# Kernel tuning notes

Measured on AMD Instinct MI355X. Metric: run time of the kernel, lower is better.

## Reference

```python
import jax, jax.numpy as jnp
import numpy as np

B, S, I, Hd = 64, 512, 512, 1024


def setup_inputs() -> dict:
    key = jax.random.key(0)
    ks = jax.random.split(key, 13)
    stdv = 1.0 / np.sqrt(Hd)
    u = lambda k, shp: jax.random.uniform(k, shp, jnp.float32, -stdv, stdv)
    x = jax.random.normal(ks[0], (B, S, I), jnp.float32)
    names = {}
    i = 1
    for g in ('1', '2', '3', '4'):
        names['X' + g] = u(ks[i], (I, Hd)); i += 1
        names['H' + g] = u(ks[i], (Hd, Hd)); i += 1
        names['b' + g] = u(ks[i], (Hd,)); i += 1
    return dict(x=x, **names)


def _lstm_forward(x, X1, H1, b1, X2, H2, b2, X3, H3, b3, X4, H4, b4):
    # Fuse the four input projections into one GEMM; math identical to
    # computing each x_t @ Xk + bk separately (slices of the concat).
    Xcat = jnp.concatenate([X1, X2, X3, X4], axis=1)          # [I, 4H]
    Hcat = jnp.concatenate([H1, H2, H3, H4], axis=1)          # [H, 4H]
    bcat = jnp.concatenate([b1, b2, b3, b4])                  # [4H]
    xg = jnp.einsum('bsi,ig->bsg', x, Xcat) + bcat            # [B, S, 4H]
    xg = jnp.swapaxes(xg, 0, 1)                               # [S, B, 4H] for scan

    Bsz = x.shape[0]
    h0 = jnp.zeros((Bsz, Hd), x.dtype)
    c0 = jnp.zeros((Bsz, Hd), x.dtype)

    def step(carry, xg_t):
        h, c = carry
        g = xg_t + h @ Hcat                                   # [B, 4H]
        s1 = jax.nn.sigmoid(g[:, :Hd])        # forget gate
        s2 = jax.nn.sigmoid(g[:, Hd:2 * Hd])  # input gate
        t1 = jnp.tanh(g[:, 2 * Hd:3 * Hd])    # candidate
        s3 = jax.nn.sigmoid(g[:, 3 * Hd:])    # output gate
        c = c * s1 + s2 * t1
        h = jnp.tanh(c) * s3
        return (h, c), h

    _, hs = jax.lax.scan(step, (h0, c0), xg)                  # hs: [S, B, H]
    return jnp.swapaxes(hs, 0, 1)                             # [B, S, H]


def reference(x, X1, H1, b1, X2, H2, b2, X3, H3, b3, X4, H4, b4):
    return _lstm_forward(x, X1, H1, b1, X2, H2, b2, X3, H3, b3, X4, H4, b4)
```

## Files before the change

### kernel.cpp

```cpp
#include <hip/hip_runtime.h>
#include <stdint.h>
#include <stddef.h>

typedef __attribute__((ext_vector_type(8))) short bf16x8;
typedef __attribute__((ext_vector_type(4))) float f32x4;

#define NBLK 128
#define NTHR 512
#define S_LEN 512
#define HD   1024
#define IDIM 512

#define MFMA16 __builtin_amdgcn_mfma_f32_16x16x32_bf16

__device__ __forceinline__ float bf2f(uint16_t u){
  union { uint32_t i; float f; } v; v.i = ((uint32_t)u) << 16; return v.f;
}
__device__ __forceinline__ uint16_t f2bf(float f){
  union { float f; uint32_t i; } v; v.f = f;
  uint32_t r = v.i + 0x7fffu + ((v.i >> 16) & 1u);
  return (uint16_t)(r >> 16);
}
__device__ __forceinline__ float sigm(float x){ return 1.0f / (1.0f + __expf(-x)); }
__device__ __forceinline__ float tanh_(float x){
  float t = fminf(fmaxf(2.0f * x, -30.0f), 30.0f);
  float e = __expf(t);
  return (e - 1.0f) / (e + 1.0f);
}

__device__ __forceinline__ void split8(const float* p, bf16x8& hi8, bf16x8& lo8){
  const float4 a = *(const float4*)p;
  const float4 b = *(const float4*)(p + 4);
  float v[8] = {a.x, a.y, a.z, a.w, b.x, b.y, b.z, b.w};
  #pragma unroll
  for (int j = 0; j < 8; ++j){
    uint16_t h = f2bf(v[j]);
    hi8[j] = (short)h;
    lo8[j] = (short)f2bf(v[j] - bf2f(h));
  }
}

__device__ __forceinline__ void cload16(const uint16_t* p, bf16x8& d){
  asm volatile("global_load_dwordx4 %0, %1, off sc0 sc1" : "=v"(d) : "v"(p));
}
__device__ __forceinline__ void cstore16b(uint16_t* p, uint32_t v){
  asm volatile("global_store_short %0, %1, off sc0 sc1" :: "v"(p), "v"(v) : "memory");
}

__global__ void __launch_bounds__(NTHR, 2) lstm_persist(
    const float* __restrict__ x,
    const float* __restrict__ X1, const float* __restrict__ H1, const float* __restrict__ b1,
    const float* __restrict__ X2, const float* __restrict__ H2, const float* __restrict__ b2,
    const float* __restrict__ X3, const float* __restrict__ H3, const float* __restrict__ b3,
    const float* __restrict__ X4, const float* __restrict__ H4, const float* __restrict__ b4,
    float* __restrict__ out, uint16_t* hbhi, uint16_t* hblo, int* done)
{
  __shared__ float part[8][64][36];
  const int tid  = threadIdx.x;
  const int w    = tid >> 6;
  const int L    = tid & 63;
  const int c    = L & 15;
  const int quad = L >> 4;
  const int cc   = c & 7;
  const int f    = blockIdx.x;
  const int colh = f * 8 + cc;
  const bool hiHalf = (c >= 8);

  const float* W0 = hiHalf ? H2 : H1;
  const float* W1 = hiHalf ? H4 : H3;
  const float* V0 = hiHalf ? X2 : X1;
  const float* V1 = hiHalf ? X4 : X3;
  const float bias0 = (hiHalf ? b2 : b1)[colh];
  const float bias1 = (hiHalf ? b4 : b3)[colh];

  bf16x8 BhH0[4], BhL0[4], BhH1[4], BhL1[4];
  #pragma unroll
  for (int kk = 0; kk < 4; ++kk){
    const int kb = w*128 + kk*32 + quad*8;
    bf16x8 h0, l0, h1, l1;
    #pragma unroll
    for (int j = 0; j < 8; ++j){
      float w0 = W0[(size_t)(kb + j)*HD + colh];
      uint16_t a = f2bf(w0); h0[j] = (short)a; l0[j] = (short)f2bf(w0 - bf2f(a));
      float w1 = W1[(size_t)(kb + j)*HD + colh];
      uint16_t b_ = f2bf(w1); h1[j] = (short)b_; l1[j] = (short)f2bf(w1 - bf2f(b_));
    }
    BhH0[kk] = h0; BhL0[kk] = l0; BhH1[kk] = h1; BhL1[kk] = l1;
  }
  bf16x8 BxH0[2], BxL0[2], BxH1[2], BxL1[2];
  #pragma unroll
  for (int kk = 0; kk < 2; ++kk){
    const int kb = w*64 + kk*32 + quad*8;
    bf16x8 h0, l0, h1, l1;
    #pragma unroll
    for (int j = 0; j < 8; ++j){
      float w0 = V0[(size_t)(kb + j)*HD + colh];
      uint16_t a = f2bf(w0); h0[j] = (short)a; l0[j] = (short)f2bf(w0 - bf2f(a));
      float w1 = V1[(size_t)(kb + j)*HD + colh];
      uint16_t b_ = f2bf(w1); h1[j] = (short)b_; l1[j] = (short)f2bf(w1 - bf2f(b_));
    }
    BxH0[kk] = h0; BxL0[kk] = l0; BxH1[kk] = h1; BxL1[kk] = l1;
  }

  float cst[2] = {0.f, 0.f};

  #pragma unroll 1
  for (int t = 0; t < S_LEN; ++t){
    const int p = t & 1;
    f32x4 acc0[4], acc1[4];
    #pragma unroll
    for (int m = 0; m < 4; ++m){
      acc0[m] = (f32x4){0.f,0.f,0.f,0.f};
      acc1[m] = (f32x4){0.f,0.f,0.f,0.f};
    }

    #pragma unroll
    for (int kk = 0; kk < 2; ++kk){
      #pragma unroll
      for (int m = 0; m < 4; ++m){
        const float* xp = x + ((size_t)(16*m + c)*S_LEN + t)*IDIM + w*64 + kk*32 + quad*8;
        bf16x8 Ah, Al; split8(xp, Ah, Al);
        acc0[m] = MFMA16(Ah, BxH0[kk], acc0[m], 0, 0, 0);
        acc0[m] = MFMA16(Al, BxH0[kk], acc0[m], 0, 0, 0);
        acc0[m] = MFMA16(Ah, BxL0[kk], acc0[m], 0, 0, 0);
        acc1[m] = MFMA16(Ah, BxH1[kk], acc1[m], 0, 0, 0);
        acc1[m] = MFMA16(Al, BxH1[kk], acc1[m], 0, 0, 0);
        acc1[m] = MFMA16(Ah, BxL1[kk], acc1[m], 0, 0, 0);
      }
    }

    if (t > 0){
      if (tid < NBLK){
        while (__hip_atomic_load(&done[tid*32], __ATOMIC_RELAXED, __HIP_MEMORY_SCOPE_AGENT) < t)
          __builtin_amdgcn_s_sleep(1);
      }
      __syncthreads();
    }

    const uint16_t* hbH = hbhi + (size_t)p * (64*HD);
    const uint16_t* hbL = hblo + (size_t)p * (64*HD);
    {
      bf16x8 AH[2][4], AL[2][4];
      #define H_OFF(m, kk) ((size_t)(16*(m) + c)*HD + w*128 + (kk)*32 + quad*8)
      #define ISSUE_M(buf, m) do { \
        _Pragma("unroll") \
        for (int kk = 0; kk < 4; ++kk){ \
          cload16(hbH + H_OFF(m, kk), AH[buf][kk]); \
          cload16(hbL + H_OFF(m, kk), AL[buf][kk]); \
        } } while(0)

      asm volatile("s_waitcnt vmcnt(0)" ::: "memory");
      ISSUE_M(0, 0);
      #pragma unroll
      for (int m = 0; m < 4; ++m){
        const int buf = m & 1;
        if (m < 3){
          ISSUE_M(buf ^ 1, m + 1);
          asm volatile("s_waitcnt vmcnt(8)" ::: "memory");
        } else {
          asm volatile("s_waitcnt vmcnt(0)" ::: "memory");
        }
        __builtin_amdgcn_sched_barrier(0);
        #pragma unroll
        for (int kk = 0; kk < 4; ++kk){
          acc0[m] = MFMA16(AH[buf][kk], BhH0[kk], acc0[m], 0, 0, 0);
          acc0[m] = MFMA16(AL[buf][kk], BhH0[kk], acc0[m], 0, 0, 0);
          acc0[m] = MFMA16(AH[buf][kk], BhL0[kk], acc0[m], 0, 0, 0);
          acc1[m] = MFMA16(AH[buf][kk], BhH1[kk], acc1[m], 0, 0, 0);
          acc1[m] = MFMA16(AL[buf][kk], BhH1[kk], acc1[m], 0, 0, 0);
          acc1[m] = MFMA16(AH[buf][kk], BhL1[kk], acc1[m], 0, 0, 0);
        }
      }
      #undef ISSUE_M
      #undef H_OFF
    }

    #pragma unroll
    for (int m = 0; m < 4; ++m){
      #pragma unroll
      for (int r = 0; r < 4; ++r){
        part[w][16*m + quad*4 + r][c]      = acc0[m][r];
        part[w][16*m + quad*4 + r][16 + c] = acc1[m][r];
      }
    }
    __syncthreads();

    float g0[2], g1[2];
    #pragma unroll
    for (int r2 = 0; r2 < 2; ++r2){
      const int row = 8*w + quad*2 + r2;
      float a = bias0, b = bias1;
      #pragma unroll
      for (int ww = 0; ww < 8; ++ww){
        a += part[ww][row][c];
        b += part[ww][row][16 + c];
      }
      g0[r2] = a; g1[r2] = b;
    }

    uint16_t* hwH = hbhi + (size_t)(p^1) * (64*HD);
    uint16_t* hwL = hblo + (size_t)(p^1) * (64*HD);
    float hv[2];
    #pragma unroll
    for (int r2 = 0; r2 < 2; ++r2){
      float gf = g0[r2];
      float gi = __shfl_xor(g0[r2], 8, 64);
      float gc = g1[r2];
      float go = __shfl_xor(g1[r2], 8, 64);
      float cn = cst[r2] * sigm(gf) + sigm(gi) * tanh_(gc);
      cst[r2] = cn;
      hv[r2] = tanh_(cn) * sigm(go);
    }
    if (!hiHalf){
      #pragma unroll
      for (int r2 = 0; r2 < 2; ++r2){
        const int batch = 8*w + quad*2 + r2;
        uint16_t hh = f2bf(hv[r2]);
        uint16_t hl = f2bf(hv[r2] - bf2f(hh));
        cstore16b(hwH + (size_t)batch*HD + colh, (uint32_t)hh);
        cstore16b(hwL + (size_t)batch*HD + colh, (uint32_t)hl);
      }
    }

    asm volatile("s_waitcnt vmcnt(0)" ::: "memory");
    __syncthreads();
    if (tid == 0)
      __hip_atomic_store(&done[f*32], t + 1, __ATOMIC_RELAXED, __HIP_MEMORY_SCOPE_AGENT);

    if (!hiHalf){
      #pragma unroll
      for (int r2 = 0; r2 < 2; ++r2){
        const int batch = 8*w + quad*2 + r2;
        __builtin_nontemporal_store(hv[r2], &out[(size_t)(batch*S_LEN + t)*HD + colh]);
      }
    }
  }
}

extern "C" void kernel_launch(void* const* d_in, const int* in_sizes, int n_in,
                              void* d_out, int out_size, void* d_ws, size_t ws_size,
                              hipStream_t stream) {
  const float* x  = (const float*)d_in[0];
  const float* X1 = (const float*)d_in[1];
  const float* H1 = (const float*)d_in[2];
  const float* b1 = (const float*)d_in[3];
  const float* X2 = (const float*)d_in[4];
  const float* H2 = (const float*)d_in[5];
  const float* b2 = (const float*)d_in[6];
  const float* X3 = (const float*)d_in[7];
  const float* H3 = (const float*)d_in[8];
  const float* b3 = (const float*)d_in[9];
  const float* X4 = (const float*)d_in[10];
  const float* H4 = (const float*)d_in[11];
  const float* b4 = (const float*)d_in[12];
  float* out = (float*)d_out;

  uint16_t* hbhi = (uint16_t*)d_ws;
  uint16_t* hblo = (uint16_t*)((char*)d_ws + 262144);
  int* done      = (int*)((char*)d_ws + 524288);
  hipMemsetAsync(d_ws, 0, 524288 + 16384, stream);

  hipLaunchKernelGGL(lstm_persist, dim3(NBLK), dim3(NTHR), 0, stream,
                     x, X1, H1, b1, X2, H2, b2, X3, H3, b3, X4, H4, b4,
                     out, hbhi, hblo, done);
}
```

Measured before the change: 7.554 ms.

## Move input projection after barrier and interleave x loads with h-loads pipeline

The x-projection MFMAs, which do not depend on h, move from before the inter-block wait to after it. Their x loads are now issued by hand and interleaved with the double-buffered h loads and recurrent MFMAs, so both load streams share one vmcnt-driven pipeline. The apparent aim is to hide global load latency inside the critical path after the wait. The trade-off is that x-projection work that used to overlap with waiting on other blocks now sits on the serial path after the barrier, and register pressure rises. The spin sleep interval is also doubled.

```diff
diff --git a/kernel.cpp b/kernel.cpp
--- a/kernel.cpp
+++ b/kernel.cpp
@@ -28,10 +28,9 @@
   return (e - 1.0f) / (e + 1.0f);
 }
 
-__device__ __forceinline__ void split8(const float* p, bf16x8& hi8, bf16x8& lo8){
-  const float4 a = *(const float4*)p;
-  const float4 b = *(const float4*)(p + 4);
-  float v[8] = {a.x, a.y, a.z, a.w, b.x, b.y, b.z, b.w};
+__device__ __forceinline__ void split8v(const f32x4& a, const f32x4& b,
+                                        bf16x8& hi8, bf16x8& lo8){
+  float v[8] = {a[0], a[1], a[2], a[3], b[0], b[1], b[2], b[3]};
   #pragma unroll
   for (int j = 0; j < 8; ++j){
     uint16_t h = f2bf(v[j]);
@@ -43,9 +42,17 @@
 __device__ __forceinline__ void cload16(const uint16_t* p, bf16x8& d){
   asm volatile("global_load_dwordx4 %0, %1, off sc0 sc1" : "=v"(d) : "v"(p));
 }
+__device__ __forceinline__ void nload16(const float* p, f32x4& d){
+  asm volatile("global_load_dwordx4 %0, %1, off" : "=v"(d) : "v"(p));
+}
 __device__ __forceinline__ void cstore16b(uint16_t* p, uint32_t v){
   asm volatile("global_store_short %0, %1, off sc0 sc1" :: "v"(p), "v"(v) : "memory");
 }
+
+#define WAITV(n) do { \
+    asm volatile("s_waitcnt vmcnt(" #n ")" ::: "memory"); \
+    __builtin_amdgcn_sched_barrier(0); \
+  } while (0)
 
 __global__ void __launch_bounds__(NTHR, 2) lstm_persist(
     const float* __restrict__ x,
@@ -114,75 +121,98 @@
       acc1[m] = (f32x4){0.f,0.f,0.f,0.f};
     }
 
-    #pragma unroll
-    for (int kk = 0; kk < 2; ++kk){
-      #pragma unroll
-      for (int m = 0; m < 4; ++m){
-        const float* xp = x + ((size_t)(16*m + c)*S_LEN + t)*IDIM + w*64 + kk*32 + quad*8;
-        bf16x8 Ah, Al; split8(xp, Ah, Al);
-        acc0[m] = MFMA16(Ah, BxH0[kk], acc0[m], 0, 0, 0);
-        acc0[m] = MFMA16(Al, BxH0[kk], acc0[m], 0, 0, 0);
-        acc0[m] = MFMA16(Ah, BxL0[kk], acc0[m], 0, 0, 0);
-        acc1[m] = MFMA16(Ah, BxH1[kk], acc1[m], 0, 0, 0);
-        acc1[m] = MFMA16(Al, BxH1[kk], acc1[m], 0, 0, 0);
-        acc1[m] = MFMA16(Ah, BxL1[kk], acc1[m], 0, 0, 0);
-      }
-    }
-
     if (t > 0){
       if (tid < NBLK){
         while (__hip_atomic_load(&done[tid*32], __ATOMIC_RELAXED, __HIP_MEMORY_SCOPE_AGENT) < t)
-          __builtin_amdgcn_s_sleep(1);
+          __builtin_amdgcn_s_sleep(2);
       }
       __syncthreads();
     }
 
     const uint16_t* hbH = hbhi + (size_t)p * (64*HD);
     const uint16_t* hbL = hblo + (size_t)p * (64*HD);
-    {
-      bf16x8 AH[2][4], AL[2][4];
-      #define H_OFF(m, kk) ((size_t)(16*(m) + c)*HD + w*128 + (kk)*32 + quad*8)
-      #define ISSUE_M(buf, m) do { \
-        _Pragma("unroll") \
-        for (int kk = 0; kk < 4; ++kk){ \
-          cload16(hbH + H_OFF(m, kk), AH[buf][kk]); \
-          cload16(hbL + H_OFF(m, kk), AL[buf][kk]); \
-        } } while(0)
-
-      asm volatile("s_waitcnt vmcnt(0)" ::: "memory");
-      ISSUE_M(0, 0);
-      #pragma unroll
-      for (int m = 0; m < 4; ++m){
-        const int buf = m & 1;
-        if (m < 3){
-          ISSUE_M(buf ^ 1, m + 1);
-          asm volatile("s_waitcnt vmcnt(8)" ::: "memory");
-        } else {
-          asm volatile("s_waitcnt vmcnt(0)" ::: "memory");
-        }
-        __builtin_amdgcn_sched_barrier(0);
-        #pragma unroll
-        for (int kk = 0; kk < 4; ++kk){
-          acc0[m] = MFMA16(AH[buf][kk], BhH0[kk], acc0[m], 0, 0, 0);
-          acc0[m] = MFMA16(AL[buf][kk], BhH0[kk], acc0[m], 0, 0, 0);
-          acc0[m] = MFMA16(AH[buf][kk], BhL0[kk], acc0[m], 0, 0, 0);
-          acc1[m] = MFMA16(AH[buf][kk], BhH1[kk], acc1[m], 0, 0, 0);
-          acc1[m] = MFMA16(AL[buf][kk], BhH1[kk], acc1[m], 0, 0, 0);
-          acc1[m] = MFMA16(AH[buf][kk], BhL1[kk], acc1[m], 0, 0, 0);
-        }
-      }
-      #undef ISSUE_M
-      #undef H_OFF
-    }
-
-    #pragma unroll
-    for (int m = 0; m < 4; ++m){
-      #pragma unroll
-      for (int r = 0; r < 4; ++r){
-        part[w][16*m + quad*4 + r][c]      = acc0[m][r];
-        part[w][16*m + quad*4 + r][16 + c] = acc1[m][r];
-      }
-    }
+
+    bf16x8 AH[2][4], AL[2][4];
+    f32x4  xr[2][2][2];
+
+    #define ISSUE_H(buf, m) do { \
+      _Pragma("unroll") \
+      for (int kk = 0; kk < 4; ++kk){ \
+        const size_t off = (size_t)(16*(m) + c)*HD + w*128 + kk*32 + quad*8; \
+        cload16(hbH + off, AH[buf][kk]); \
+        cload16(hbL + off, AL[buf][kk]); \
+      } } while(0)
+
+    #define ISSUE_X(buf, m) do { \
+      _Pragma("unroll") \
+      for (int kk = 0; kk < 2; ++kk){ \
+        const float* xp = x + ((size_t)(16*(m) + c)*S_LEN + t)*IDIM + w*64 + kk*32 + quad*8; \
+        nload16(xp,     xr[buf][kk][0]); \
+        nload16(xp + 4, xr[buf][kk][1]); \
+      } } while(0)
+
+    #define MFMA_H(buf, m) do { \
+      _Pragma("unroll") \
+      for (int kk = 0; kk < 4; ++kk){ \
+        acc0[m] = MFMA16(AH[buf][kk], BhH0[kk], acc0[m], 0, 0, 0); \
+        acc0[m] = MFMA16(AL[buf][kk], BhH0[kk], acc0[m], 0, 0, 0); \
+        acc0[m] = MFMA16(AH[buf][kk], BhL0[kk], acc0[m], 0, 0, 0); \
+        acc1[m] = MFMA16(AH[buf][kk], BhH1[kk], acc1[m], 0, 0, 0); \
+        acc1[m] = MFMA16(AL[buf][kk], BhH1[kk], acc1[m], 0, 0, 0); \
+        acc1[m] = MFMA16(AH[buf][kk], BhL1[kk], acc1[m], 0, 0, 0); \
+      } } while(0)
+
+    #define XWORK(buf, m) do { \
+      _Pragma("unroll") \
+      for (int kk = 0; kk < 2; ++kk){ \
+        bf16x8 Ah, Al; split8v(xr[buf][kk][0], xr[buf][kk][1], Ah, Al); \
+        acc0[m] = MFMA16(Ah, BxH0[kk], acc0[m], 0, 0, 0); \
+        acc0[m] = MFMA16(Al, BxH0[kk], acc0[m], 0, 0, 0); \
+        acc0[m] = MFMA16(Ah, BxL0[kk], acc0[m], 0, 0, 0); \
+        acc1[m] = MFMA16(Ah, BxH1[kk], acc1[m], 0, 0, 0); \
+        acc1[m] = MFMA16(Al, BxH1[kk], acc1[m], 0, 0, 0); \
+        acc1[m] = MFMA16(Ah, BxL1[kk], acc1[m], 0, 0, 0); \
+      } } while(0)
+
+    #define STASH(m) do { \
+      _Pragma("unroll") \
+      for (int r = 0; r < 4; ++r){ \
+        part[w][16*(m) + quad*4 + r][c]      = acc0[m][r]; \
+        part[w][16*(m) + quad*4 + r][16 + c] = acc1[m][r]; \
+      } } while(0)
+
+    WAITV(0);
+    ISSUE_H(0, 0);
+    ISSUE_H(1, 1);
+    ISSUE_X(0, 0);
+    ISSUE_X(1, 1);
+    WAITV(16);
+    MFMA_H(0, 0);
+    ISSUE_H(0, 2);
+    WAITV(16);
+    MFMA_H(1, 1);
+    ISSUE_H(1, 3);
+    WAITV(16);
+    XWORK(0, 0);
+    XWORK(1, 1);
+    STASH(0); STASH(1);
+    WAITV(8);
+    MFMA_H(0, 2);
+    ISSUE_X(0, 2);
+    ISSUE_X(1, 3);
+    WAITV(8);
+    MFMA_H(1, 3);
+    WAITV(0);
+    XWORK(0, 2);
+    XWORK(1, 3);
+    STASH(2); STASH(3);
+
+    #undef ISSUE_H
+    #undef ISSUE_X
+    #undef MFMA_H
+    #undef XWORK
+    #undef STASH
+
     __syncthreads();
 
     float g0[2], g1[2];
```

Result: slower. 7.833 ms (+3.7%).

## Exchange hidden state through fp32 output buffer instead of split bf16 workspace

Applied to the files above, without the earlier changes.

Each step now reads the previous hidden state straight from the fp32 output tensor (row t-1) and splits it into hi/lo bf16 on the fly. The separate double-buffered hi/lo bf16 workspace and the duplicate output store are removed. The output store becomes a single coherent store issued before the done flag. This cuts the store count and the extra workspace traffic per step, at the cost of extra split ALU work on the critical path. The loads are plain (non-sc) global loads of data written by other blocks, so freshness depends on cache behaviour, and the spin sleep interval is also raised.

```diff
diff --git a/kernel.cpp b/kernel.cpp
--- a/kernel.cpp
+++ b/kernel.cpp
@@ -39,13 +39,28 @@
     lo8[j] = (short)f2bf(v[j] - bf2f(h));
   }
 }
-
-__device__ __forceinline__ void cload16(const uint16_t* p, bf16x8& d){
-  asm volatile("global_load_dwordx4 %0, %1, off sc0 sc1" : "=v"(d) : "v"(p));
-}
-__device__ __forceinline__ void cstore16b(uint16_t* p, uint32_t v){
-  asm volatile("global_store_short %0, %1, off sc0 sc1" :: "v"(p), "v"(v) : "memory");
-}
+__device__ __forceinline__ void split8v(const f32x4& a, const f32x4& b,
+                                        bf16x8& hi8, bf16x8& lo8){
+  float v[8] = {a[0], a[1], a[2], a[3], b[0], b[1], b[2], b[3]};
+  #pragma unroll
+  for (int j = 0; j < 8; ++j){
+    uint16_t h = f2bf(v[j]);
+    hi8[j] = (short)h;
+    lo8[j] = (short)f2bf(v[j] - bf2f(h));
+  }
+}
+
+__device__ __forceinline__ void nload16(const float* p, f32x4& d){
+  asm volatile("global_load_dwordx4 %0, %1, off" : "=v"(d) : "v"(p));
+}
+__device__ __forceinline__ void fstore_sc(float* p, float v){
+  asm volatile("global_store_dword %0, %1, off sc0 sc1" :: "v"(p), "v"(v) : "memory");
+}
+
+#define WAITV(n) do { \
+    asm volatile("s_waitcnt vmcnt(" #n ")" ::: "memory"); \
+    __builtin_amdgcn_sched_barrier(0); \
+  } while (0)
 
 __global__ void __launch_bounds__(NTHR, 2) lstm_persist(
     const float* __restrict__ x,
@@ -53,7 +68,7 @@
     const float* __restrict__ X2, const float* __restrict__ H2, const float* __restrict__ b2,
     const float* __restrict__ X3, const float* __restrict__ H3, const float* __restrict__ b3,
     const float* __restrict__ X4, const float* __restrict__ H4, const float* __restrict__ b4,
-    float* __restrict__ out, uint16_t* hbhi, uint16_t* hblo, int* done)
+    float* __restrict__ out, int* done)
 {
   __shared__ float part[8][64][36];
   const int tid  = threadIdx.x;
@@ -106,7 +121,6 @@
 
   #pragma unroll 1
   for (int t = 0; t < S_LEN; ++t){
-    const int p = t & 1;
     f32x4 acc0[4], acc1[4];
     #pragma unroll
     for (int m = 0; m < 4; ++m){
@@ -132,47 +146,45 @@
     if (t > 0){
       if (tid < NBLK){
         while (__hip_atomic_load(&done[tid*32], __ATOMIC_RELAXED, __HIP_MEMORY_SCOPE_AGENT) < t)
-          __builtin_amdgcn_s_sleep(1);
+          __builtin_amdgcn_s_sleep(2);
       }
       __syncthreads();
-    }
-
-    const uint16_t* hbH = hbhi + (size_t)p * (64*HD);
-    const uint16_t* hbL = hblo + (size_t)p * (64*HD);
-    {
-      bf16x8 AH[2][4], AL[2][4];
-      #define H_OFF(m, kk) ((size_t)(16*(m) + c)*HD + w*128 + (kk)*32 + quad*8)
+
+      f32x4 raw[2][4][2];
+      #define H_PTR(m, kk) (out + ((size_t)(16*(m) + c)*S_LEN + (t-1))*HD \
+                                + w*128 + (kk)*32 + quad*8)
       #define ISSUE_M(buf, m) do { \
         _Pragma("unroll") \
         for (int kk = 0; kk < 4; ++kk){ \
-          cload16(hbH + H_OFF(m, kk), AH[buf][kk]); \
-          cload16(hbL + H_OFF(m, kk), AL[buf][kk]); \
+          nload16(H_PTR(m, kk),     raw[buf][kk][0]); \
+          nload16(H_PTR(m, kk) + 4, raw[buf][kk][1]); \
         } } while(0)
 
-      asm volatile("s_waitcnt vmcnt(0)" ::: "memory");
+      WAITV(0);
       ISSUE_M(0, 0);
       #pragma unroll
       for (int m = 0; m < 4; ++m){
         const int buf = m & 1;
         if (m < 3){
           ISSUE_M(buf ^ 1, m + 1);
-          asm volatile("s_waitcnt vmcnt(8)" ::: "memory");
+          WAITV(8);
         } else {
-          asm volatile("s_waitcnt vmcnt(0)" ::: "memory");
+          WAITV(0);
         }
-        __builtin_amdgcn_sched_barrier(0);
         #pragma unroll
         for (int kk = 0; kk < 4; ++kk){
-          acc0[m] = MFMA16(AH[buf][kk], BhH0[kk], acc0[m], 0, 0, 0);
-          acc0[m] = MFMA16(AL[buf][kk], BhH0[kk], acc0[m], 0, 0, 0);
-          acc0[m] = MFMA16(AH[buf][kk], BhL0[kk], acc0[m], 0, 0, 0);
-          acc1[m] = MFMA16(AH[buf][kk], BhH1[kk], acc1[m], 0, 0, 0);
-          acc1[m] = MFMA16(AL[buf][kk], BhH1[kk], acc1[m], 0, 0, 0);
-          acc1[m] = MFMA16(AH[buf][kk], BhL1[kk], acc1[m], 0, 0, 0);
+          bf16x8 Ah, Al;
+          split8v(raw[buf][kk][0], raw[buf][kk][1], Ah, Al);
+          acc0[m] = MFMA16(Ah, BhH0[kk], acc0[m], 0, 0, 0);
+          acc0[m] = MFMA16(Al, BhH0[kk], acc0[m], 0, 0, 0);
+          acc0[m] = MFMA16(Ah, BhL0[kk], acc0[m], 0, 0, 0);
+          acc1[m] = MFMA16(Ah, BhH1[kk], acc1[m], 0, 0, 0);
+          acc1[m] = MFMA16(Al, BhH1[kk], acc1[m], 0, 0, 0);
+          acc1[m] = MFMA16(Ah, BhL1[kk], acc1[m], 0, 0, 0);
         }
       }
       #undef ISSUE_M
-      #undef H_OFF
+      #undef H_PTR
     }
 
     #pragma unroll
@@ -198,8 +210,6 @@
       g0[r2] = a; g1[r2] = b;
     }
 
-    uint16_t* hwH = hbhi + (size_t)(p^1) * (64*HD);
-    uint16_t* hwL = hblo + (size_t)(p^1) * (64*HD);
     float hv[2];
     #pragma unroll
     for (int r2 = 0; r2 < 2; ++r2){
@@ -211,14 +221,12 @@
       cst[r2] = cn;
       hv[r2] = tanh_(cn) * sigm(go);
     }
+
     if (!hiHalf){
       #pragma unroll
       for (int r2 = 0; r2 < 2; ++r2){
         const int batch = 8*w + quad*2 + r2;
-        uint16_t hh = f2bf(hv[r2]);
-        uint16_t hl = f2bf(hv[r2] - bf2f(hh));
-        cstore16b(hwH + (size_t)batch*HD + colh, (uint32_t)hh);
-        cstore16b(hwL + (size_t)batch*HD + colh, (uint32_t)hl);
+        fstore_sc(&out[(size_t)(batch*S_LEN + t)*HD + colh], hv[r2]);
       }
     }
 
@@ -226,14 +234,6 @@
     __syncthreads();
     if (tid == 0)
       __hip_atomic_store(&done[f*32], t + 1, __ATOMIC_RELAXED, __HIP_MEMORY_SCOPE_AGENT);
-
-    if (!hiHalf){
-      #pragma unroll
-      for (int r2 = 0; r2 < 2; ++r2){
-        const int batch = 8*w + quad*2 + r2;
-        __builtin_nontemporal_store(hv[r2], &out[(size_t)(batch*S_LEN + t)*HD + colh]);
-      }
-    }
   }
 }
 
@@ -255,12 +255,10 @@
   const float* b4 = (const float*)d_in[12];
   float* out = (float*)d_out;
 
-  uint16_t* hbhi = (uint16_t*)d_ws;
-  uint16_t* hblo = (uint16_t*)((char*)d_ws + 262144);
-  int* done      = (int*)((char*)d_ws + 524288);
-  hipMemsetAsync(d_ws, 0, 524288 + 16384, stream);
+  int* done = (int*)d_ws;
+  hipMemsetAsync(d_ws, 0, 16384, stream);
 
   hipLaunchKernelGGL(lstm_persist, dim3(NBLK), dim3(NTHR), 0, stream,
                      x, X1, H1, b1, X2, H2, b2, X3, H3, b3, X4, H4, b4,
-                     out, hbhi, hblo, done);
-}
+                     out, done);
+}
```

After: 8.268 ms. +9.5%, slower.
